# Performance work log

Measured on AMD Instinct MI355X. Metric: run time of the kernel, lower is better.

## Reference

```python
import jax, jax.numpy as jnp
import numpy as np

B, S, DIN, DOUT = 4, 2048, 4096, 11008


def setup_inputs() -> dict:
    key = jax.random.key(0)
    k1, k2, k3, k4 = jax.random.split(key, 4)
    x = jax.random.normal(k1, (B, S, DIN), dtype=jnp.float32)
    # signed int8 quantized weights, stored as int32 for portability
    Wq = jax.random.randint(k2, (DOUT, DIN), -127, 128, dtype=jnp.int32)
    # per-output-channel scales (positive, clamped >= 1e-8 as in from_float)
    scale = jnp.maximum(jax.random.uniform(k3, (DOUT,), dtype=jnp.float32) * 0.02, 1e-8)
    b = jax.random.normal(k4, (DOUT,), dtype=jnp.float32)
    return {"x": x, "Wq": Wq, "scale": scale, "b": b}


def reference(x, Wq, scale, b):
    # dequantize: W[o, i] = Wq[o, i] * scale[o]
    W = Wq.astype(x.dtype) * scale[:, None].astype(x.dtype)
    # y = x @ W.T + bias  (leading dims flattened implicitly by einsum)
    y = jnp.einsum('bsi,oi->bso', x, W) + b.astype(x.dtype)
    # act_type == 'gelu' -> act_id = 1 (exact GELU, matching torch default)
    y = jax.nn.gelu(y, approximate=False)
    return y
```

## Files before the change

kernel.cpp:

```cpp
#include <hip/hip_runtime.h>
#include <cstdint>
#include <cstddef>


#define Msz 8192
#define Nsz 11008
#define Ksz 4096

#define TM 256
#define TN 256
#define TK 128
#define NT (Ksz / TK)
#define NI (NT / 2)
#define HALF (128 * TK)
#define NWG ((Msz / TM) * (Nsz / TN))
#define CPX (NWG / 8)

#define BM 128
#define BN 128

typedef __attribute__((ext_vector_type(4))) int int4v;
typedef __attribute__((ext_vector_type(8))) short short8;
typedef __attribute__((ext_vector_type(4))) float floatx4;

__device__ __forceinline__ void async16(const void* g, void* l) {
  __builtin_amdgcn_global_load_lds(
      (const __attribute__((address_space(1))) void*)g,
      (__attribute__((address_space(3))) void*)l, 16, 0, 0);
}

__global__ __launch_bounds__(256) void quant_x(
    const float* __restrict__ x, signed char* __restrict__ xq,
    float* __restrict__ qs) {
  const int row = blockIdx.x;
  const int tid = threadIdx.x;
  const int lane = tid & 63;
  const int wave = tid >> 6;
  const float4* xr = (const float4*)(x + (size_t)row * Ksz);

  float4 v[4];
  float m = 0.f;
#pragma unroll
  for (int t = 0; t < 4; ++t) {
    v[t] = xr[tid + t * 256];
    m = fmaxf(m, fmaxf(fmaxf(fabsf(v[t].x), fabsf(v[t].y)),
                       fmaxf(fabsf(v[t].z), fabsf(v[t].w))));
  }
#pragma unroll
  for (int o = 32; o > 0; o >>= 1) m = fmaxf(m, __shfl_down(m, o));
  __shared__ float sm[4];
  if (lane == 0) sm[wave] = m;
  __syncthreads();
  const float am = fmaxf(fmaxf(sm[0], sm[1]), fmaxf(sm[2], sm[3]));
  const float rs = am > 0.f ? 127.0f / am : 0.f;
  if (tid == 0) qs[row] = am * (1.0f / 127.0f);

  unsigned* outd = (unsigned*)(xq + (size_t)row * Ksz);
#pragma unroll
  for (int t = 0; t < 4; ++t) {
    int q0 = __float2int_rn(fminf(fmaxf(v[t].x * rs, -127.f), 127.f));
    int q1 = __float2int_rn(fminf(fmaxf(v[t].y * rs, -127.f), 127.f));
    int q2 = __float2int_rn(fminf(fmaxf(v[t].z * rs, -127.f), 127.f));
    int q3 = __float2int_rn(fminf(fmaxf(v[t].w * rs, -127.f), 127.f));
    outd[tid + t * 256] = (unsigned)(q0 & 255) | ((unsigned)(q1 & 255) << 8) |
                          ((unsigned)(q2 & 255) << 16) | ((unsigned)q3 << 24);
  }
}

__global__ __launch_bounds__(256) void pack_w(const int4* __restrict__ w,
                                              unsigned* __restrict__ o) {
  const unsigned gid = blockIdx.x * 256 + threadIdx.x;
  const unsigned stride = 11008u * 256u;
#pragma unroll
  for (int t = 0; t < 4; ++t) {
    const unsigned idx = gid + t * stride;
    const int4 a = w[idx];
    o[idx] = (unsigned)(a.x & 255) | ((unsigned)(a.y & 255) << 8) |
             ((unsigned)(a.z & 255) << 16) | ((unsigned)a.w << 24);
  }
}

__device__ __forceinline__ void stage_half(signed char* dst,
                                           const signed char* src, int grow0,
                                           int kt, int tid) {
  const int c = tid & 7;
  const int k0 = kt * TK;
#pragma unroll
  for (int rho = 0; rho < 2; ++rho) {
    const int rl = rho * 64 + (tid >> 3);
    async16(src + (size_t)(grow0 + rl) * Ksz + k0 + ((c ^ (rl & 7)) << 4),
            dst + rho * 8192 + tid * 16);
  }
}

__device__ __forceinline__ int4v ldfrag(const signed char* s, int row,
                                        int slot) {
  return *(const int4v*)(s + row * TK + (((slot) ^ (row & 7)) << 4));
}

#define PHASE(b, q, LOADB, SDST, GSRC, GROW0, KT, VM)                        \
  {                                                                          \
    int4v afr[2][2];                                                         \
    _Pragma("unroll") for (int ii = 0; ii < 2; ++ii) {                       \
      const int ar = wr * 128 + ((2 * (q) + ii) << 4) + (lane & 15);         \
      _Pragma("unroll") for (int kk = 0; kk < 2; ++kk)                       \
          afr[ii][kk] = ldfrag(sA[b], ar, kk * 4 + (lane >> 4));             \
    }                                                                        \
    if (LOADB) {                                                             \
      _Pragma("unroll") for (int jj = 0; jj < 4; ++jj) {                     \
        const int br = wc * 64 + (jj << 4) + (lane & 15);                    \
        _Pragma("unroll") for (int kk = 0; kk < 2; ++kk)                     \
            bfr[jj][kk] = ldfrag(sB[b], br, kk * 4 + (lane >> 4));           \
      }                                                                      \
    }                                                                        \
    stage_half(SDST, GSRC, GROW0, KT, tid);                                  \
    if (LOADB) asm volatile("s_waitcnt lgkmcnt(8)" ::: "memory");            \
    __builtin_amdgcn_s_barrier();                                            \
    asm volatile("s_waitcnt lgkmcnt(0)" ::: "memory");                       \
    __builtin_amdgcn_s_setprio(1);                                           \
    _Pragma("unroll") for (int kk = 0; kk < 2; ++kk)                         \
        _Pragma("unroll") for (int ii = 0; ii < 2; ++ii)                     \
            _Pragma("unroll") for (int jj = 0; jj < 4; ++jj)                 \
                acc[2 * (q) + ii][jj] =                                      \
                    __builtin_amdgcn_mfma_i32_16x16x64_i8(                   \
                        afr[ii][kk], bfr[jj][kk], acc[2 * (q) + ii][jj], 0,  \
                        0, 0);                                               \
    __builtin_amdgcn_s_setprio(0);                                           \
    if (VM) asm volatile("s_waitcnt vmcnt(4)" ::: "memory");                 \
    __builtin_amdgcn_s_barrier();                                            \
  }

__global__ __launch_bounds__(512, 2) void gemm_i8(
    const signed char* __restrict__ A8,
    const signed char* __restrict__ B8,
    const float* __restrict__ qs,
    const float* __restrict__ scale, const float* __restrict__ bias,
    float* __restrict__ out) {
  __shared__ signed char sA[2][TM * TK];
  __shared__ signed char sB[2][TN * TK];

  const int tid = threadIdx.x;
  const int wave = tid >> 6;
  const int lane = tid & 63;
  const int wr = wave >> 2;
  const int wc = wave & 3;

  const int bid = blockIdx.x;
  const int swz = (bid & 7) * CPX + (bid >> 3);
  const int bm0 = (swz & 31) * TM;
  const int bn0 = (swz >> 5) * TN;

  int4v acc[8][4];
#pragma unroll
  for (int i = 0; i < 8; ++i)
#pragma unroll
    for (int j = 0; j < 4; ++j) acc[i][j] = (int4v)0;
  int4v bfr[4][2];

  stage_half(sA[0], A8, bm0, 0, tid);
  stage_half(sA[0] + HALF, A8, bm0 + 128, 0, tid);
  stage_half(sB[0], B8, bn0, 0, tid);
  stage_half(sB[0] + HALF, B8, bn0 + 128, 0, tid);
  stage_half(sB[1], B8, bn0, 1, tid);
  stage_half(sB[1] + HALF, B8, bn0 + 128, 1, tid);
  asm volatile("s_waitcnt vmcnt(4)" ::: "memory");
  __builtin_amdgcn_s_barrier();

  for (int j = 0; j < NI; ++j) {
    const int tA1 = 2 * j + 1;
    const int tB2 = (2 * j + 2 < NT) ? 2 * j + 2 : NT - 1;
    const int tB3 = (2 * j + 3 < NT) ? 2 * j + 3 : NT - 1;
    PHASE(0, 0, true, sA[1], A8, bm0, tA1, false)
    PHASE(0, 1, false, sA[1] + HALF, A8, bm0 + 128, tA1, false)
    PHASE(0, 2, false, sB[0], B8, bn0, tB2, false)
    PHASE(0, 3, false, sB[0] + HALF, B8, bn0 + 128, tB2, true)
    PHASE(1, 0, true, sA[0], A8, bm0, tB2, false)
    PHASE(1, 1, false, sA[0] + HALF, A8, bm0 + 128, tB2, false)
    PHASE(1, 2, false, sB[1], B8, bn0, tB3, false)
    PHASE(1, 3, false, sB[1] + HALF, B8, bn0 + 128, tB3, true)
  }
  asm volatile("s_waitcnt vmcnt(0)" ::: "memory");

  float sc[4], bb[4];
#pragma unroll
  for (int jj = 0; jj < 4; ++jj) {
    const int col = bn0 + wc * 64 + jj * 16 + (lane & 15);
    sc[jj] = scale[col];
    bb[jj] = bias[col];
  }
#pragma unroll
  for (int i = 0; i < 8; ++i) {
    const int row0 = bm0 + wr * 128 + i * 16 + (lane >> 4) * 4;
    float qv[4];
#pragma unroll
    for (int r = 0; r < 4; ++r) qv[r] = qs[row0 + r];
#pragma unroll
    for (int jj = 0; jj < 4; ++jj) {
      const int col = bn0 + wc * 64 + jj * 16 + (lane & 15);
#pragma unroll
      for (int r = 0; r < 4; ++r) {
        float v = (float)acc[i][jj][r] * (qv[r] * sc[jj]) + bb[jj];
        v = 0.5f * v * (1.0f + erff(v * 0.7071067811865476f));
        out[(size_t)(row0 + r) * Nsz + col] = v;
      }
    }
  }
}

__device__ __forceinline__ unsigned int f2bf(float f) {
  unsigned int u = __builtin_bit_cast(unsigned int, f);
  unsigned int r = u + 0x7FFFu + ((u >> 16) & 1u);
  return r >> 16;
}

__global__ __launch_bounds__(256) void gemm_bf16_inline(
    const float* __restrict__ Af, const int* __restrict__ Bi,
    const float* __restrict__ scale, const float* __restrict__ bias,
    float* __restrict__ out) {
  __shared__ unsigned short sA[BM * 32];
  __shared__ unsigned short sB[BN * 32];
  const int tid = threadIdx.x;
  const int wave = tid >> 6;
  const int lane = tid & 63;
  const int bn0 = blockIdx.x * BN;
  const int bm0 = blockIdx.y * BM;
  const int mw = (wave >> 1) * 64;
  const int nw = (wave & 1) * 64;
  floatx4 acc[4][4];
#pragma unroll
  for (int i = 0; i < 4; ++i)
#pragma unroll
    for (int j = 0; j < 4; ++j) acc[i][j] = (floatx4)0.f;
  for (int k0 = 0; k0 < Ksz; k0 += 32) {
#pragma unroll
    for (int it = 0; it < 4; ++it) {
      const int f = tid + it * 256;
      const int row = f >> 3;
      const int c4 = (f & 7) * 4;
      const float4 v = *(const float4*)(Af + (size_t)(bm0 + row) * Ksz + k0 + c4);
      uint2 p;
      p.x = f2bf(v.x) | (f2bf(v.y) << 16);
      p.y = f2bf(v.z) | (f2bf(v.w) << 16);
      *(uint2*)&sA[row * 32 + c4] = p;
      const int4 w2 = *(const int4*)(Bi + (size_t)(bn0 + row) * Ksz + k0 + c4);
      uint2 q;
      q.x = f2bf((float)w2.x) | (f2bf((float)w2.y) << 16);
      q.y = f2bf((float)w2.z) | (f2bf((float)w2.w) << 16);
      *(uint2*)&sB[row * 32 + c4] = q;
    }
    __syncthreads();
    short8 af[4], bfr[4];
    const int kof2 = (lane >> 4) * 8;
#pragma unroll
    for (int i = 0; i < 4; ++i) {
      af[i] = *(const short8*)&sA[(mw + i * 16 + (lane & 15)) * 32 + kof2];
      bfr[i] = *(const short8*)&sB[(nw + i * 16 + (lane & 15)) * 32 + kof2];
    }
#pragma unroll
    for (int i = 0; i < 4; ++i)
#pragma unroll
      for (int j = 0; j < 4; ++j)
        acc[i][j] =
            __builtin_amdgcn_mfma_f32_16x16x32_bf16(af[i], bfr[j], acc[i][j], 0, 0, 0);
    __syncthreads();
  }
#pragma unroll
  for (int j = 0; j < 4; ++j) {
    const int col = bn0 + nw + j * 16 + (lane & 15);
    const float s = scale[col];
    const float bb = bias[col];
#pragma unroll
    for (int i = 0; i < 4; ++i) {
      const int row0 = bm0 + mw + i * 16 + (lane >> 4) * 4;
#pragma unroll
      for (int r = 0; r < 4; ++r) {
        float v = acc[i][j][r] * s + bb;
        v = 0.5f * v * (1.0f + erff(v * 0.7071067811865476f));
        out[(size_t)(row0 + r) * Nsz + col] = v;
      }
    }
  }
}

extern "C" void kernel_launch(void* const* d_in, const int* in_sizes, int n_in,
                              void* d_out, int out_size, void* d_ws, size_t ws_size,
                              hipStream_t stream) {
  const float* x = (const float*)d_in[0];
  const int* Wq = (const int*)d_in[1];
  const float* scale = (const float*)d_in[2];
  const float* bias = (const float*)d_in[3];
  float* out = (float*)d_out;

  const size_t nx = (size_t)Msz * Ksz;
  const size_t nwq = (size_t)Nsz * Ksz;
  const size_t need = nx + nwq + Msz * sizeof(float);

  if (ws_size >= need) {
    signed char* xq = (signed char*)d_ws;
    signed char* wp = xq + nx;
    float* qsd = (float*)(wp + nwq);
    quant_x<<<dim3(Msz), dim3(256), 0, stream>>>(x, xq, qsd);
    pack_w<<<dim3((unsigned)(nwq / (16 * 256))), dim3(256), 0, stream>>>(
        (const int4*)Wq, (unsigned*)wp);
    gemm_i8<<<dim3(NWG), dim3(512), 0, stream>>>(xq, wp, qsd, scale, bias, out);
  } else {
    dim3 grid(Nsz / BN, Msz / BM);
    gemm_bf16_inline<<<grid, dim3(256), 0, stream>>>(x, Wq, scale, bias, out);
  }
}
```

Baseline: 1.137 ms.

## Register double-buffer LDS fragments in int8 GEMM and merge prep kernels

Restructures the int8 GEMM main loop so A and B fragments for the next phase are read from LDS into alternate register sets while the current phase's MFMAs run. Precomputed read and stage addresses replace per-phase index math, and sched_barrier plus tuned waitcnts pin the ordering. It also merges the activation quantization and weight packing kernels into one launch to save a launch and the gap between them. This costs extra registers for the doubled fragment sets, which risks spills or lower occupancy, and hand-counted waitcnt values that must match the number of loads in flight.

Result: faster. 1.009 ms (-11.3%).

```diff
diff --git a/kernel.cpp b/kernel.cpp
--- a/kernel.cpp
+++ b/kernel.cpp
@@ -12,7 +12,6 @@
 #define TK 128
 #define NT (Ksz / TK)
 #define NI (NT / 2)
-#define HALF (128 * TK)
 #define NWG ((Msz / TM) * (Nsz / TN))
 #define CPX (NWG / 8)
 
@@ -29,105 +28,102 @@
       (__attribute__((address_space(3))) void*)l, 16, 0, 0);
 }
 
-__global__ __launch_bounds__(256) void quant_x(
-    const float* __restrict__ x, signed char* __restrict__ xq,
+__global__ __launch_bounds__(256) void prep(
+    const float* __restrict__ x, const int4* __restrict__ w,
+    signed char* __restrict__ xq, unsigned* __restrict__ wp,
     float* __restrict__ qs) {
-  const int row = blockIdx.x;
   const int tid = threadIdx.x;
-  const int lane = tid & 63;
-  const int wave = tid >> 6;
-  const float4* xr = (const float4*)(x + (size_t)row * Ksz);
-
-  float4 v[4];
-  float m = 0.f;
-#pragma unroll
-  for (int t = 0; t < 4; ++t) {
-    v[t] = xr[tid + t * 256];
-    m = fmaxf(m, fmaxf(fmaxf(fabsf(v[t].x), fabsf(v[t].y)),
-                       fmaxf(fabsf(v[t].z), fabsf(v[t].w))));
-  }
-#pragma unroll
-  for (int o = 32; o > 0; o >>= 1) m = fmaxf(m, __shfl_down(m, o));
-  __shared__ float sm[4];
-  if (lane == 0) sm[wave] = m;
-  __syncthreads();
-  const float am = fmaxf(fmaxf(sm[0], sm[1]), fmaxf(sm[2], sm[3]));
-  const float rs = am > 0.f ? 127.0f / am : 0.f;
-  if (tid == 0) qs[row] = am * (1.0f / 127.0f);
-
-  unsigned* outd = (unsigned*)(xq + (size_t)row * Ksz);
-#pragma unroll
-  for (int t = 0; t < 4; ++t) {
-    int q0 = __float2int_rn(fminf(fmaxf(v[t].x * rs, -127.f), 127.f));
-    int q1 = __float2int_rn(fminf(fmaxf(v[t].y * rs, -127.f), 127.f));
-    int q2 = __float2int_rn(fminf(fmaxf(v[t].z * rs, -127.f), 127.f));
-    int q3 = __float2int_rn(fminf(fmaxf(v[t].w * rs, -127.f), 127.f));
-    outd[tid + t * 256] = (unsigned)(q0 & 255) | ((unsigned)(q1 & 255) << 8) |
-                          ((unsigned)(q2 & 255) << 16) | ((unsigned)q3 << 24);
-  }
-}
-
-__global__ __launch_bounds__(256) void pack_w(const int4* __restrict__ w,
-                                              unsigned* __restrict__ o) {
-  const unsigned gid = blockIdx.x * 256 + threadIdx.x;
-  const unsigned stride = 11008u * 256u;
-#pragma unroll
-  for (int t = 0; t < 4; ++t) {
-    const unsigned idx = gid + t * stride;
-    const int4 a = w[idx];
-    o[idx] = (unsigned)(a.x & 255) | ((unsigned)(a.y & 255) << 8) |
-             ((unsigned)(a.z & 255) << 16) | ((unsigned)a.w << 24);
-  }
-}
-
-__device__ __forceinline__ void stage_half(signed char* dst,
-                                           const signed char* src, int grow0,
-                                           int kt, int tid) {
-  const int c = tid & 7;
-  const int k0 = kt * TK;
-#pragma unroll
-  for (int rho = 0; rho < 2; ++rho) {
-    const int rl = rho * 64 + (tid >> 3);
-    async16(src + (size_t)(grow0 + rl) * Ksz + k0 + ((c ^ (rl & 7)) << 4),
-            dst + rho * 8192 + tid * 16);
-  }
-}
-
-__device__ __forceinline__ int4v ldfrag(const signed char* s, int row,
-                                        int slot) {
-  return *(const int4v*)(s + row * TK + (((slot) ^ (row & 7)) << 4));
-}
-
-#define PHASE(b, q, LOADB, SDST, GSRC, GROW0, KT, VM)                        \
-  {                                                                          \
-    int4v afr[2][2];                                                         \
-    _Pragma("unroll") for (int ii = 0; ii < 2; ++ii) {                       \
-      const int ar = wr * 128 + ((2 * (q) + ii) << 4) + (lane & 15);         \
-      _Pragma("unroll") for (int kk = 0; kk < 2; ++kk)                       \
-          afr[ii][kk] = ldfrag(sA[b], ar, kk * 4 + (lane >> 4));             \
-    }                                                                        \
-    if (LOADB) {                                                             \
-      _Pragma("unroll") for (int jj = 0; jj < 4; ++jj) {                     \
-        const int br = wc * 64 + (jj << 4) + (lane & 15);                    \
-        _Pragma("unroll") for (int kk = 0; kk < 2; ++kk)                     \
-            bfr[jj][kk] = ldfrag(sB[b], br, kk * 4 + (lane >> 4));           \
-      }                                                                      \
-    }                                                                        \
-    stage_half(SDST, GSRC, GROW0, KT, tid);                                  \
-    if (LOADB) asm volatile("s_waitcnt lgkmcnt(8)" ::: "memory");            \
-    __builtin_amdgcn_s_barrier();                                            \
-    asm volatile("s_waitcnt lgkmcnt(0)" ::: "memory");                       \
-    __builtin_amdgcn_s_setprio(1);                                           \
-    _Pragma("unroll") for (int kk = 0; kk < 2; ++kk)                         \
-        _Pragma("unroll") for (int ii = 0; ii < 2; ++ii)                     \
-            _Pragma("unroll") for (int jj = 0; jj < 4; ++jj)                 \
-                acc[2 * (q) + ii][jj] =                                      \
-                    __builtin_amdgcn_mfma_i32_16x16x64_i8(                   \
-                        afr[ii][kk], bfr[jj][kk], acc[2 * (q) + ii][jj], 0,  \
-                        0, 0);                                               \
-    __builtin_amdgcn_s_setprio(0);                                           \
-    if (VM) asm volatile("s_waitcnt vmcnt(4)" ::: "memory");                 \
-    __builtin_amdgcn_s_barrier();                                            \
+  if (blockIdx.x < 8192) {
+    const int row = blockIdx.x;
+    const int lane = tid & 63;
+    const int wave = tid >> 6;
+    const float4* xr = (const float4*)(x + (size_t)row * Ksz);
+    float4 v[4];
+    float m = 0.f;
+#pragma unroll
+    for (int t = 0; t < 4; ++t) {
+      v[t] = xr[tid + t * 256];
+      m = fmaxf(m, fmaxf(fmaxf(fabsf(v[t].x), fabsf(v[t].y)),
+                         fmaxf(fabsf(v[t].z), fabsf(v[t].w))));
+    }
+#pragma unroll
+    for (int o = 32; o > 0; o >>= 1) m = fmaxf(m, __shfl_down(m, o));
+    __shared__ float sm[4];
+    if (lane == 0) sm[wave] = m;
+    __syncthreads();
+    const float am = fmaxf(fmaxf(sm[0], sm[1]), fmaxf(sm[2], sm[3]));
+    const float rs = am > 0.f ? 127.0f / am : 0.f;
+    if (tid == 0) qs[row] = am * (1.0f / 127.0f);
+    unsigned* outd = (unsigned*)(xq + (size_t)row * Ksz);
+#pragma unroll
+    for (int t = 0; t < 4; ++t) {
+      int q0 = __float2int_rn(fminf(fmaxf(v[t].x * rs, -127.f), 127.f));
+      int q1 = __float2int_rn(fminf(fmaxf(v[t].y * rs, -127.f), 127.f));
+      int q2 = __float2int_rn(fminf(fmaxf(v[t].z * rs, -127.f), 127.f));
+      int q3 = __float2int_rn(fminf(fmaxf(v[t].w * rs, -127.f), 127.f));
+      outd[tid + t * 256] = (unsigned)(q0 & 255) | ((unsigned)(q1 & 255) << 8) |
+                            ((unsigned)(q2 & 255) << 16) | ((unsigned)q3 << 24);
+    }
+  } else {
+    const unsigned gid = (blockIdx.x - 8192) * 256 + tid;
+    const unsigned stride = 11008u * 256u;
+#pragma unroll
+    for (int t = 0; t < 4; ++t) {
+      const unsigned idx = gid + t * stride;
+      const int4 a = w[idx];
+      wp[idx] = (unsigned)(a.x & 255) | ((unsigned)(a.y & 255) << 8) |
+                ((unsigned)(a.z & 255) << 16) | ((unsigned)a.w << 24);
+    }
+  }
+}
+
+
+#define RD_A(DST, BUF, Q)                                                      \
+  DST[0] = *(const int4v*)(ldsb + aRd0 + ((BUF)*32768 + (2*(Q)+0)*2048));      \
+  DST[1] = *(const int4v*)(ldsb + aRd1 + ((BUF)*32768 + (2*(Q)+0)*2048));      \
+  DST[2] = *(const int4v*)(ldsb + aRd0 + ((BUF)*32768 + (2*(Q)+1)*2048));      \
+  DST[3] = *(const int4v*)(ldsb + aRd1 + ((BUF)*32768 + (2*(Q)+1)*2048));
+
+#define RD_B(DST, BUF)                                                         \
+  _Pragma("unroll") for (int jj = 0; jj < 4; ++jj) {                           \
+    DST[jj*2+0] = *(const int4v*)(ldsb + bRd0 + ((BUF)*32768 + jj*2048));      \
+    DST[jj*2+1] = *(const int4v*)(ldsb + bRd1 + ((BUF)*32768 + jj*2048));      \
+  }
+
+#define MM(Q, A, B)                                                            \
+  __builtin_amdgcn_s_setprio(1);                                               \
+  _Pragma("unroll") for (int kk = 0; kk < 2; ++kk)                             \
+  _Pragma("unroll") for (int ii = 0; ii < 2; ++ii)                             \
+  _Pragma("unroll") for (int jj = 0; jj < 4; ++jj)                             \
+    acc[2*(Q)+ii][jj] = __builtin_amdgcn_mfma_i32_16x16x64_i8(                 \
+        A[ii*2+kk], B[jj*2+kk], acc[2*(Q)+ii][jj], 0, 0, 0);                   \
+  __builtin_amdgcn_s_setprio(0);
+
+#define ST_A(BUF, Q, KT)                                                       \
+  async16(aG + (size_t)(KT)*128 + (size_t)(Q)*131072,                          \
+          ldsb + aStD + ((BUF)*32768 + (Q)*4096));
+
+#define ST_B(BUF, HH, KT)                                                      \
+  async16(bG + (size_t)(HH)*524288 + (size_t)(KT)*128,                         \
+          ldsb + bStD + (65536 + (BUF)*32768 + (HH)*16384));                   \
+  async16(bG2 + (size_t)(HH)*524288 + (size_t)(KT)*128,                        \
+          ldsb + bStD + (65536 + (BUF)*32768 + (HH)*16384 + 8192));
+
+#define SB __builtin_amdgcn_sched_barrier(0)
+#define VMW(N) asm volatile("s_waitcnt vmcnt(" #N ")" ::: "memory")
+#define LGW(N) asm volatile("s_waitcnt lgkmcnt(" #N ")" ::: "memory")
+
+#define PH(RD_CODE, STAGE_CODE, LGN, Q, ASET, BSET)                            \
+  {                                                                            \
+    RD_CODE;                                                                   \
+    STAGE_CODE;                                                                \
+    LGW(LGN);                                                                  \
+    SB;                                                                        \
+    MM(Q, ASET, BSET);                                                         \
+    SB;                                                                        \
+    VMW(8);                                                                    \
+    __builtin_amdgcn_s_barrier();                                              \
+    SB;                                                                        \
   }
 
 __global__ __launch_bounds__(512, 2) void gemm_i8(
@@ -136,8 +132,7 @@
     const float* __restrict__ qs,
     const float* __restrict__ scale, const float* __restrict__ bias,
     float* __restrict__ out) {
-  __shared__ signed char sA[2][TM * TK];
-  __shared__ signed char sB[2][TN * TK];
+  __shared__ signed char ldsb[131072];
 
   const int tid = threadIdx.x;
   const int wave = tid >> 6;
@@ -150,53 +145,77 @@
   const int bm0 = (swz & 31) * TM;
   const int bn0 = (swz >> 5) * TN;
 
+  const int lane15 = lane & 15, lane7 = lane & 7, lg = lane >> 4;
+  const int kkp0 = ((0 * 4 + lg) ^ lane7) << 4;
+  const int kkp1 = ((1 * 4 + lg) ^ lane7) << 4;
+  const int aRd0 = wr * 16384 + lane15 * 128 + kkp0;
+  const int aRd1 = wr * 16384 + lane15 * 128 + kkp1;
+  const int bRd0 = 65536 + wc * 8192 + lane15 * 128 + kkp0;
+  const int bRd1 = 65536 + wc * 8192 + lane15 * 128 + kkp1;
+
+  const int sA_ = (tid & 255) >> 3;
+  const signed char* aG =
+      A8 + (size_t)(bm0 + (tid >> 8) * 128 + sA_) * Ksz +
+      (((tid & 7) ^ (sA_ & 7)) << 4);
+  const int aStD = (tid >> 8) * 16384 + (tid & 255) * 16;
+  const int sB_ = tid >> 3;
+  const signed char* bG =
+      B8 + (size_t)(bn0 + sB_) * Ksz + (((tid & 7) ^ (sB_ & 7)) << 4);
+  const signed char* bG2 =
+      B8 + (size_t)(bn0 + 64 + sB_) * Ksz + (((tid & 7) ^ (sB_ & 7)) << 4);
+  const int bStD = tid * 16;
+
   int4v acc[8][4];
 #pragma unroll
   for (int i = 0; i < 8; ++i)
 #pragma unroll
     for (int j = 0; j < 4; ++j) acc[i][j] = (int4v)0;
-  int4v bfr[4][2];
-
-  stage_half(sA[0], A8, bm0, 0, tid);
-  stage_half(sA[0] + HALF, A8, bm0 + 128, 0, tid);
-  stage_half(sB[0], B8, bn0, 0, tid);
-  stage_half(sB[0] + HALF, B8, bn0 + 128, 0, tid);
-  stage_half(sB[1], B8, bn0, 1, tid);
-  stage_half(sB[1] + HALF, B8, bn0 + 128, 1, tid);
-  asm volatile("s_waitcnt vmcnt(4)" ::: "memory");
+  int4v afA[4], afB[4], bfA[8], bfB[8];
+
+  ST_A(0, 0, 0) ST_B(0, 0, 0)
+  ST_A(0, 1, 0) ST_B(0, 1, 0)
+  ST_A(0, 2, 0)
+  ST_A(0, 3, 0)
+  ST_A(1, 0, 1) ST_B(1, 0, 1)
+  ST_A(1, 1, 1) ST_B(1, 1, 1)
+  ST_A(1, 2, 1)
+  VMW(7);
   __builtin_amdgcn_s_barrier();
+  SB;
+  RD_A(afA, 0, 0)
+  RD_B(bfA, 0)
 
   for (int j = 0; j < NI; ++j) {
-    const int tA1 = 2 * j + 1;
-    const int tB2 = (2 * j + 2 < NT) ? 2 * j + 2 : NT - 1;
-    const int tB3 = (2 * j + 3 < NT) ? 2 * j + 3 : NT - 1;
-    PHASE(0, 0, true, sA[1], A8, bm0, tA1, false)
-    PHASE(0, 1, false, sA[1] + HALF, A8, bm0 + 128, tA1, false)
-    PHASE(0, 2, false, sB[0], B8, bn0, tB2, false)
-    PHASE(0, 3, false, sB[0] + HALF, B8, bn0 + 128, tB2, true)
-    PHASE(1, 0, true, sA[0], A8, bm0, tB2, false)
-    PHASE(1, 1, false, sA[0] + HALF, A8, bm0 + 128, tB2, false)
-    PHASE(1, 2, false, sB[1], B8, bn0, tB3, false)
-    PHASE(1, 3, false, sB[1] + HALF, B8, bn0 + 128, tB3, true)
-  }
-  asm volatile("s_waitcnt vmcnt(0)" ::: "memory");
+    const int t1 = 2 * j + 1;
+    const int t2 = (2 * j + 2 < NT) ? 2 * j + 2 : NT - 1;
+    const int t3 = (2 * j + 3 < NT) ? 2 * j + 3 : NT - 1;
+    PH(RD_A(afB, 0, 1), ST_A(1, 3, t1), 4, 0, afA, bfA)
+    PH(RD_A(afA, 0, 2), ST_A(0, 0, t2) ST_B(0, 0, t2), 4, 1, afB, bfA)
+    PH(RD_A(afB, 0, 3), ST_A(0, 1, t2) ST_B(0, 1, t2), 4, 2, afA, bfA)
+    PH(RD_A(afA, 1, 0) RD_B(bfB, 1), ST_A(0, 2, t2), 12, 3, afB, bfA)
+    PH(RD_A(afB, 1, 1), ST_A(0, 3, t2), 4, 0, afA, bfB)
+    PH(RD_A(afA, 1, 2), ST_A(1, 0, t3) ST_B(1, 0, t3), 4, 1, afB, bfB)
+    PH(RD_A(afB, 1, 3), ST_A(1, 1, t3) ST_B(1, 1, t3), 4, 2, afA, bfB)
+    PH(RD_A(afA, 0, 0) RD_B(bfA, 0), ST_A(1, 2, t3), 12, 3, afB, bfB)
+  }
+  asm volatile("s_waitcnt vmcnt(0) lgkmcnt(0)" ::: "memory");
 
   float sc[4], bb[4];
 #pragma unroll
   for (int jj = 0; jj < 4; ++jj) {
-    const int col = bn0 + wc * 64 + jj * 16 + (lane & 15);
+    const int col = bn0 + wc * 64 + jj * 16 + lane15;
     sc[jj] = scale[col];
     bb[jj] = bias[col];
   }
 #pragma unroll
   for (int i = 0; i < 8; ++i) {
-    const int row0 = bm0 + wr * 128 + i * 16 + (lane >> 4) * 4;
+    const int row0 = bm0 + wr * 128 + i * 16 + lg * 4;
     float qv[4];
 #pragma unroll
     for (int r = 0; r < 4; ++r) qv[r] = qs[row0 + r];
 #pragma unroll
     for (int jj = 0; jj < 4; ++jj) {
-      const int col = bn0 + wc * 64 + jj * 16 + (lane & 15);
+      const int col = bn0 + wc * 64 + jj * 16 + lane15;
 #pragma unroll
       for (int r = 0; r < 4; ++r) {
         float v = (float)acc[i][jj][r] * (qv[r] * sc[jj]) + bb[jj];
@@ -299,9 +318,8 @@
     signed char* xq = (signed char*)d_ws;
     signed char* wp = xq + nx;
     float* qsd = (float*)(wp + nwq);
-    quant_x<<<dim3(Msz), dim3(256), 0, stream>>>(x, xq, qsd);
-    pack_w<<<dim3((unsigned)(nwq / (16 * 256))), dim3(256), 0, stream>>>(
-        (const int4*)Wq, (unsigned*)wp);
+    prep<<<dim3(8192 + 11008), dim3(256), 0, stream>>>(
+        x, (const int4*)Wq, xq, (unsigned*)wp, qsd);
     gemm_i8<<<dim3(NWG), dim3(512), 0, stream>>>(xq, wp, qsd, scale, bias, out);
   } else {
     dim3 grid(Nsz / BN, Msz / BM);
```
